# Kernel optimization log

Hardware: AMD Instinct MI355X
Metric: run time of the kernel (lower is better)

Reference implementation:

```python
import jax, jax.numpy as jnp
import numpy as np

N_OUT = 100000 - 1  # 99999, as hard-coded in the torch module
LEAK = 0.01         # torch LeakyReLU default slope


def setup_inputs() -> dict:
    key = jax.random.key(0)
    k1, k2, k3, k4, k5 = jax.random.split(key, 5)
    B, D = 512, 512
    H = D // 2
    x = jax.random.normal(k1, (B, D), dtype=jnp.float32)
    # torch.nn.Linear-style init scale ~ 1/sqrt(fan_in)
    w2 = jax.random.normal(k2, (H, D), dtype=jnp.float32) / np.sqrt(D)
    b2 = jax.random.normal(k3, (H,), dtype=jnp.float32) / np.sqrt(D)
    w3 = jax.random.normal(k4, (55, H), dtype=jnp.float32) / np.sqrt(H)
    b3 = jax.random.normal(k5, (55,), dtype=jnp.float32) / np.sqrt(H)
    return {"x": x, "w2": w2, "b2": b2, "w3": w3, "b3": b3}


def _digit_tables():
    # Static integer tables for i in [0, N_OUT).
    i = np.arange(N_OUT, dtype=np.int32)
    ndig = ((i >= 10).astype(np.int32) + (i >= 100) + (i >= 1000) + (i >= 10000)).astype(np.int32)
    ndig[0] = 1  # special case in the original code: i==0 -> n=1
    return jnp.asarray(i), jnp.asarray(ndig)


def reference(x, w2, b2, w3, b3):
    # tiny MLP (batched; equivalent to the per-sample torch loop)
    h = x @ w2.T + b2
    h = jnp.where(h >= 0, h, LEAK * h)          # LeakyReLU
    z = h @ w3.T + b3                            # [B, 55]
    p_len = jax.nn.softmax(z[:, :5], axis=-1)    # length distribution (5)
    p_dig = jax.nn.softmax(z[:, 5:].reshape(-1, 5, 10), axis=-1)  # 5 digit groups of 10
    x3 = jnp.concatenate([p_len, p_dig.reshape(-1, 50)], axis=-1)  # [B, 55]

    i, ndig = _digit_tables()                    # [N], [N]
    out = jnp.take(x3, ndig, axis=1)             # lead factor x3[k, n_i] -> [B, N]
    # Multiply the first n_i digit probabilities (original drops the last digit).
    for j in range(4):                           # max usable digits: n<=4
        expo = jnp.maximum(ndig - j, 0)
        d = (i // jnp.power(10, expo)) % 10      # j-th most significant digit
        idx = 5 + d + 10 * j                     # index into x3 digit groups
        factor = jnp.take(x3, idx, axis=1)       # [B, N]
        valid = (j < ndig)[None, :]
        out = out * jnp.where(valid, factor, 1.0)
    return out
```

## Files before the change

kernel.cpp:

```cpp
#include <hip/hip_runtime.h>
#include <hip/hip_bf16.h>


#define BATCH 512
#define DIM   512
#define HID   256
#define NCLS  55
#define NOUT  99999
#define LEAK  0.01f

__global__ __launch_bounds__(256) void mlp_x3_kernel(
    const float* __restrict__ x,  const float* __restrict__ w2,
    const float* __restrict__ b2, const float* __restrict__ w3,
    const float* __restrict__ b3, float* __restrict__ x3out) {
    __shared__ float xs[DIM];
    __shared__ float hs[HID];
    __shared__ float x3s[NCLS];

    const int tid  = threadIdx.x;
    const int k    = blockIdx.x;
    const int wave = tid >> 6;
    const int lane = tid & 63;

    xs[tid]       = x[(size_t)k * DIM + tid];
    xs[tid + 256] = x[(size_t)k * DIM + tid + 256];
    __syncthreads();

    {
        float4 xv0 = ((const float4*)xs)[lane];
        float4 xv1 = ((const float4*)xs)[lane + 64];
        float  biasv = b2[wave * 64 + lane];
        float  acc = 0.f;
#pragma unroll 4
        for (int t = 0; t < 64; ++t) {
            const int n = wave * 64 + t;
            const float4* w2r = (const float4*)(w2 + (size_t)n * DIM);
            float4 a = w2r[lane];
            float4 b = w2r[lane + 64];
            float s = a.x * xv0.x + a.y * xv0.y + a.z * xv0.z + a.w * xv0.w
                    + b.x * xv1.x + b.y * xv1.y + b.z * xv1.z + b.w * xv1.w;
#pragma unroll
            for (int off = 1; off < 64; off <<= 1) s += __shfl_xor(s, off, 64);
            if (lane == t) acc = s;
        }
        float hv = acc + biasv;
        hs[wave * 64 + lane] = (hv >= 0.f) ? hv : LEAK * hv;
    }
    __syncthreads();

    {
        float4 hv = ((const float4*)hs)[lane];
        for (int o = wave; o < NCLS; o += 4) {
            const float4* w3r = (const float4*)(w3 + (size_t)o * HID);
            float4 w = w3r[lane];
            float s = w.x * hv.x + w.y * hv.y + w.z * hv.z + w.w * hv.w;
#pragma unroll
            for (int off = 1; off < 64; off <<= 1) s += __shfl_xor(s, off, 64);
            if (lane == 0) x3s[o] = s + b3[o];
        }
    }
    __syncthreads();

    if (tid < 6) {
        int off = (tid == 0) ? 0 : 5 + 10 * (tid - 1);
        int len = (tid == 0) ? 5 : 10;
        float m = -1e30f;
        for (int u = 0; u < len; ++u) m = fmaxf(m, x3s[off + u]);
        float s = 0.f;
        for (int u = 0; u < len; ++u) {
            float e = __expf(x3s[off + u] - m);
            x3s[off + u] = e;
            s += e;
        }
        float inv = 1.f / s;
        for (int u = 0; u < len; ++u) x3s[off + u] *= inv;
    }
    __syncthreads();

    if (tid < NCLS) x3out[k * NCLS + tid] = x3s[tid];
}

__device__ __forceinline__ float Vj(
    unsigned j, const float* __restrict__ T4A, const float* __restrict__ T3A,
    const float* __restrict__ T2A, const float* __restrict__ B4,
    const float* __restrict__ B3,  const float* __restrict__ A1b) {
    if (j >= 1000u) { unsigned q = j / 100u; return T4A[q] * B4[j - q * 100u]; }
    if (j >= 100u)  { unsigned q = j / 10u;  return T3A[q] * B3[j - q * 10u]; }
    if (j >= 10u)   return T2A[j];
    return A1b[j];
}

__global__ __launch_bounds__(256) void expand_kernel(
    const float* __restrict__ x3g, float* __restrict__ out) {
    __shared__ float T4A[100], T3A[100], T2A[100], B4[100];
    __shared__ float B3[16], A1b[16];
    __shared__ float x3s[NCLS];

    const int tid = threadIdx.x;
    const int k   = blockIdx.x >> 3;
    const int s   = blockIdx.x & 7;

    if (tid < NCLS) x3s[tid] = x3g[k * NCLS + tid];
    __syncthreads();

    if (tid < 100) {
        int hi = tid / 10, lo = tid % 10;
        float pp = x3s[5 + hi] * x3s[15 + lo];
        T4A[tid] = x3s[4] * pp;
        T3A[tid] = x3s[3] * pp;
        T2A[tid] = x3s[2] * pp;
        B4[tid]  = x3s[25 + hi] * x3s[35 + lo];
    } else if (tid < 110) {
        int d = tid - 100;
        B3[d]  = x3s[25 + d];
        A1b[d] = (d == 0) ? x3s[0] : x3s[1] * x3s[5 + d];
    }
    __syncthreads();

    const float pz = x3s[1] * x3s[5];

    const unsigned e_lo = (unsigned)s * 12500u;
    const unsigned n_el = (s == 7) ? 12499u : 12500u;
    const size_t   gbase = (size_t)k * NOUT + e_lo;
    const unsigned head = (unsigned)((4u - ((unsigned)gbase & 3u)) & 3u);
    const unsigned ng   = (n_el - head) >> 2;
    const unsigned tail0 = head + (ng << 2);

    if (tid < (int)head) {
        unsigned i = e_lo + (unsigned)tid;
        float v = Vj(i / 10u, T4A, T3A, T2A, B4, B3, A1b);
        if (i == 0u) v = pz;
        out[gbase + tid] = v;
    }
    if (tid < (int)(n_el - tail0)) {
        unsigned e = tail0 + (unsigned)tid;
        unsigned i = e_lo + e;
        out[gbase + e] = Vj(i / 10u, T4A, T3A, T2A, B4, B3, A1b);
    }

    float4* outv = (float4*)(out + gbase + head);
    for (unsigned g = tid; g < ng; g += 256) {
        unsigned i   = e_lo + head + (g << 2);
        unsigned j0  = i / 10u;
        unsigned rem = i - j0 * 10u;
        float v0 = Vj(j0, T4A, T3A, T2A, B4, B3, A1b);
        unsigned j1 = j0 + (rem >= 7u ? 1u : 0u);
        float v1 = Vj(j1, T4A, T3A, T2A, B4, B3, A1b);
        unsigned m = 10u - rem;
        float4 v;
        v.x = (i == 0u) ? pz : v0;
        v.y = (1u < m) ? v0 : v1;
        v.z = (2u < m) ? v0 : v1;
        v.w = (3u < m) ? v0 : v1;
        outv[g] = v;
    }
}

extern "C" void kernel_launch(void* const* d_in, const int* in_sizes, int n_in,
                              void* d_out, int out_size, void* d_ws, size_t ws_size,
                              hipStream_t stream) {
    const float* x  = (const float*)d_in[0];
    const float* w2 = (const float*)d_in[1];
    const float* b2 = (const float*)d_in[2];
    const float* w3 = (const float*)d_in[3];
    const float* b3 = (const float*)d_in[4];
    float* out = (float*)d_out;
    float* x3  = (float*)d_ws;

    mlp_x3_kernel<<<BATCH, 256, 0, stream>>>(x, w2, b2, w3, b3, x3);
    expand_kernel<<<BATCH * 8, 256, 0, stream>>>(x3, out);
}
```

Baseline: 238.8 us.

## Fuse MLP and expansion into one kernel with a shared-memory value table

Merges the MLP kernel and the output expansion kernel into a single launch with one 512-thread block per batch row. Each block precomputes all 10000 distinct output values into shared memory, then writes the 99999-wide row with float4 stores that read that table. This removes the second launch, the workspace round trip, and the per-element branchy lookups. In exchange the grid shrinks from 4096 blocks to 512, each block uses about 40KB of LDS, and the write-heavy phase now has fewer independent blocks to hide memory latency.

```diff
diff --git a/kernel.cpp b/kernel.cpp
--- a/kernel.cpp
+++ b/kernel.cpp
@@ -1,5 +1,4 @@
 #include <hip/hip_runtime.h>
-#include <hip/hip_bf16.h>
 
 
 #define BATCH 512
@@ -9,31 +8,32 @@
 #define NOUT  99999
 #define LEAK  0.01f
 
-__global__ __launch_bounds__(256) void mlp_x3_kernel(
+__global__ __launch_bounds__(512) void fused_mlp_expand(
     const float* __restrict__ x,  const float* __restrict__ w2,
     const float* __restrict__ b2, const float* __restrict__ w3,
-    const float* __restrict__ b3, float* __restrict__ x3out) {
+    const float* __restrict__ b3, float* __restrict__ out) {
     __shared__ float xs[DIM];
     __shared__ float hs[HID];
     __shared__ float x3s[NCLS];
+    __shared__ float AB[100];
+    __shared__ float CD[100];
+    __shared__ float VS[10004];
 
     const int tid  = threadIdx.x;
     const int k    = blockIdx.x;
     const int wave = tid >> 6;
     const int lane = tid & 63;
 
-    xs[tid]       = x[(size_t)k * DIM + tid];
-    xs[tid + 256] = x[(size_t)k * DIM + tid + 256];
+    xs[tid] = x[(size_t)k * DIM + tid];
     __syncthreads();
 
     {
         float4 xv0 = ((const float4*)xs)[lane];
         float4 xv1 = ((const float4*)xs)[lane + 64];
-        float  biasv = b2[wave * 64 + lane];
         float  acc = 0.f;
 #pragma unroll 4
-        for (int t = 0; t < 64; ++t) {
-            const int n = wave * 64 + t;
+        for (int t = 0; t < 32; ++t) {
+            const int n = wave * 32 + t;
             const float4* w2r = (const float4*)(w2 + (size_t)n * DIM);
             float4 a = w2r[lane];
             float4 b = w2r[lane + 64];
@@ -43,14 +43,16 @@
             for (int off = 1; off < 64; off <<= 1) s += __shfl_xor(s, off, 64);
             if (lane == t) acc = s;
         }
-        float hv = acc + biasv;
-        hs[wave * 64 + lane] = (hv >= 0.f) ? hv : LEAK * hv;
+        if (lane < 32) {
+            float hv = acc + b2[wave * 32 + lane];
+            hs[wave * 32 + lane] = (hv >= 0.f) ? hv : LEAK * hv;
+        }
     }
     __syncthreads();
 
     {
         float4 hv = ((const float4*)hs)[lane];
-        for (int o = wave; o < NCLS; o += 4) {
+        for (int o = wave; o < NCLS; o += 8) {
             const float4* w3r = (const float4*)(w3 + (size_t)o * HID);
             float4 w = w3r[lane];
             float s = w.x * hv.x + w.y * hv.y + w.z * hv.z + w.w * hv.w;
@@ -77,81 +79,55 @@
     }
     __syncthreads();
 
-    if (tid < NCLS) x3out[k * NCLS + tid] = x3s[tid];
-}
-
-__device__ __forceinline__ float Vj(
-    unsigned j, const float* __restrict__ T4A, const float* __restrict__ T3A,
-    const float* __restrict__ T2A, const float* __restrict__ B4,
-    const float* __restrict__ B3,  const float* __restrict__ A1b) {
-    if (j >= 1000u) { unsigned q = j / 100u; return T4A[q] * B4[j - q * 100u]; }
-    if (j >= 100u)  { unsigned q = j / 10u;  return T3A[q] * B3[j - q * 10u]; }
-    if (j >= 10u)   return T2A[j];
-    return A1b[j];
-}
-
-__global__ __launch_bounds__(256) void expand_kernel(
-    const float* __restrict__ x3g, float* __restrict__ out) {
-    __shared__ float T4A[100], T3A[100], T2A[100], B4[100];
-    __shared__ float B3[16], A1b[16];
-    __shared__ float x3s[NCLS];
-
-    const int tid = threadIdx.x;
-    const int k   = blockIdx.x >> 3;
-    const int s   = blockIdx.x & 7;
-
-    if (tid < NCLS) x3s[tid] = x3g[k * NCLS + tid];
-    __syncthreads();
-
     if (tid < 100) {
         int hi = tid / 10, lo = tid % 10;
-        float pp = x3s[5 + hi] * x3s[15 + lo];
-        T4A[tid] = x3s[4] * pp;
-        T3A[tid] = x3s[3] * pp;
-        T2A[tid] = x3s[2] * pp;
-        B4[tid]  = x3s[25 + hi] * x3s[35 + lo];
-    } else if (tid < 110) {
-        int d = tid - 100;
-        B3[d]  = x3s[25 + d];
-        A1b[d] = (d == 0) ? x3s[0] : x3s[1] * x3s[5 + d];
+        AB[tid] = x3s[5 + hi] * x3s[15 + lo];
+        CD[tid] = x3s[25 + hi] * x3s[35 + lo];
     }
     __syncthreads();
 
-    const float pz = x3s[1] * x3s[5];
+    {
+        const float A10 = x3s[0];
+        const float L1 = x3s[1], L2 = x3s[2], L3 = x3s[3], L4 = x3s[4];
+        for (int j = tid; j < 10000; j += 512) {
+            unsigned ju = (unsigned)j;
+            float v;
+            if (ju >= 1000u)      { unsigned q = ju / 100u; v = L4 * AB[q] * CD[ju - q * 100u]; }
+            else if (ju >= 100u)  { unsigned q = ju / 10u;  v = L3 * AB[q] * x3s[25 + (ju - q * 10u)]; }
+            else if (ju >= 10u)   { v = L2 * AB[ju]; }
+            else                  { v = (ju == 0u) ? A10 : L1 * x3s[5 + ju]; }
+            VS[j] = v;
+        }
+    }
+    __syncthreads();
 
-    const unsigned e_lo = (unsigned)s * 12500u;
-    const unsigned n_el = (s == 7) ? 12499u : 12500u;
-    const size_t   gbase = (size_t)k * NOUT + e_lo;
-    const unsigned head = (unsigned)((4u - ((unsigned)gbase & 3u)) & 3u);
-    const unsigned ng   = (n_el - head) >> 2;
-    const unsigned tail0 = head + (ng << 2);
+    const float  pz = x3s[1] * x3s[5];
+    const size_t rb = (size_t)k * NOUT;
+    const unsigned h     = (unsigned)((4u - (unsigned)(rb & 3)) & 3u);
+    const unsigned ng    = ((unsigned)NOUT - h) >> 2;
+    const unsigned tail0 = h + (ng << 2);
 
-    if (tid < (int)head) {
-        unsigned i = e_lo + (unsigned)tid;
-        float v = Vj(i / 10u, T4A, T3A, T2A, B4, B3, A1b);
-        if (i == 0u) v = pz;
-        out[gbase + tid] = v;
+    if (tid < (int)h) {
+        unsigned e = (unsigned)tid;
+        out[rb + e] = (e == 0u) ? pz : VS[0];
     }
-    if (tid < (int)(n_el - tail0)) {
+    if (tid < (int)((unsigned)NOUT - tail0)) {
         unsigned e = tail0 + (unsigned)tid;
-        unsigned i = e_lo + e;
-        out[gbase + e] = Vj(i / 10u, T4A, T3A, T2A, B4, B3, A1b);
+        out[rb + e] = VS[e / 10u];
     }
 
-    float4* outv = (float4*)(out + gbase + head);
-    for (unsigned g = tid; g < ng; g += 256) {
-        unsigned i   = e_lo + head + (g << 2);
-        unsigned j0  = i / 10u;
-        unsigned rem = i - j0 * 10u;
-        float v0 = Vj(j0, T4A, T3A, T2A, B4, B3, A1b);
-        unsigned j1 = j0 + (rem >= 7u ? 1u : 0u);
-        float v1 = Vj(j1, T4A, T3A, T2A, B4, B3, A1b);
-        unsigned m = 10u - rem;
+    float4* outv = (float4*)(out + rb + h);
+    for (unsigned g = tid; g < ng; g += 512) {
+        unsigned e   = h + (g << 2);
+        unsigned j   = e / 10u;
+        unsigned rem = e - j * 10u;
+        float v0 = VS[j];
+        float v1 = VS[j + 1];
         float4 v;
-        v.x = (i == 0u) ? pz : v0;
-        v.y = (1u < m) ? v0 : v1;
-        v.z = (2u < m) ? v0 : v1;
-        v.w = (3u < m) ? v0 : v1;
+        v.x = (e == 0u)  ? pz : v0;
+        v.y = (rem < 9u) ? v0 : v1;
+        v.z = (rem < 8u) ? v0 : v1;
+        v.w = (rem < 7u) ? v0 : v1;
         outv[g] = v;
     }
 }
@@ -165,8 +141,6 @@
     const float* w3 = (const float*)d_in[3];
     const float* b3 = (const float*)d_in[4];
     float* out = (float*)d_out;
-    float* x3  = (float*)d_ws;
 
-    mlp_x3_kernel<<<BATCH, 256, 0, stream>>>(x, w2, b2, w3, b3, x3);
-    expand_kernel<<<BATCH * 8, 256, 0, stream>>>(x3, out);
+    fused_mlp_expand<<<BATCH, 512, 0, stream>>>(x, w2, b2, w3, b3, out);
 }
```

New measurement: 230.2 us. -3.6%, faster.
